# Optimization experiments

Measured on AMD Instinct MI355X. Metric: run time of the kernel, lower is better.

The kernel has to match this reference:

```python
import jax, jax.numpy as jnp
import numpy as np

N, E, D, H = 100000, 1250000, 64, 128
EPS = 1e-5


def sage_bn_relu(x, src, dst, W_self, b_self, W_neigh, gamma, beta):
    # mean aggregation over in-neighbors (DGL SAGEConv 'mean')
    n = x.shape[0]
    deg = jax.ops.segment_sum(jnp.ones((src.shape[0],), x.dtype), dst, num_segments=n)
    agg = jax.ops.segment_sum(x[src], dst, num_segments=n)  # [N, d]
    neigh = agg / jnp.maximum(deg, 1.0)[:, None]             # zero in-degree -> 0
    h = x @ W_self + b_self + neigh @ W_neigh                # fc_self + fc_neigh
    # BatchNorm1d (training-mode batch statistics, biased variance)
    mu = h.mean(0)
    var = jnp.mean((h - mu) ** 2, axis=0)
    h = (h - mu) * jax.lax.rsqrt(var + EPS) * gamma + beta
    return jax.nn.relu(h)  # dropout omitted (deterministic eval)


def setup_inputs() -> dict:
    key = jax.random.key(0)
    ks = jax.random.split(key, 32)
    inp = {
        "x": jax.random.normal(ks[0], (N, D), jnp.float32),
        "src": jax.random.randint(ks[1], (E,), 0, N),
        "dst": jax.random.randint(ks[2], (E,), 0, N),
    }
    dims = [(D, H), (H, H), (H, H)]
    k = 3
    for i, (din, dout) in enumerate(dims):
        s = 1.0 / np.sqrt(din)
        inp[f"W_self{i}"] = jax.random.uniform(ks[k], (din, dout), jnp.float32, -s, s); k += 1
        inp[f"b_self{i}"] = jnp.zeros((dout,), jnp.float32)
        inp[f"W_neigh{i}"] = jax.random.uniform(ks[k], (din, dout), jnp.float32, -s, s); k += 1
        inp[f"gamma{i}"] = jnp.ones((dout,), jnp.float32)
        inp[f"beta{i}"] = jnp.zeros((dout,), jnp.float32)
    s = 1.0 / np.sqrt(H)
    inp["Wc"] = jax.random.uniform(ks[k], (H, 2), jnp.float32, -s, s)
    inp["bc"] = jnp.zeros((2,), jnp.float32)
    return inp


def reference(x, src, dst,
              W_self0, b_self0, W_neigh0, gamma0, beta0,
              W_self1, b_self1, W_neigh1, gamma1, beta1,
              W_self2, b_self2, W_neigh2, gamma2, beta2,
              Wc, bc):
    h = sage_bn_relu(x, src, dst, W_self0, b_self0, W_neigh0, gamma0, beta0)
    h = sage_bn_relu(h, src, dst, W_self1, b_self1, W_neigh1, gamma1, beta1)
    h = sage_bn_relu(h, src, dst, W_self2, b_self2, W_neigh2, gamma2, beta2)
    return h @ Wc + bc  # [N, 2]
```

## Files before the change

kernel.cpp:

```cpp
#include <hip/hip_runtime.h>


#define N_NODES 100000
#define N_EDGES 1250000
#define NB 1024
#define BSZ 98
#define CAP 1536
#define BPART 256
#define INVN (1.0f / 100000.0f)

typedef short bf16x8 __attribute__((ext_vector_type(8)));
typedef float f32x4 __attribute__((ext_vector_type(4)));
typedef unsigned short u16x8 __attribute__((ext_vector_type(8)));
typedef unsigned short u16x4 __attribute__((ext_vector_type(4)));

__device__ __forceinline__ float bf2f(unsigned short u) {
  union { unsigned int i; float f; } c; c.i = ((unsigned int)u) << 16; return c.f;
}
__device__ __forceinline__ unsigned short f2bf(float f) {
  union { float f; unsigned int i; } c; c.f = f;
  unsigned int r = (c.i + 0x7FFFu + ((c.i >> 16) & 1u)) >> 16;
  return (unsigned short)r;
}
__device__ __forceinline__ void bn_st(const float* stats, const float* gam,
                                      const float* bet, int c, float& s, float& t) {
  float sum = stats[c] + stats[256 + c] + stats[512 + c] + stats[768 + c];
  float sq  = stats[128 + c] + stats[384 + c] + stats[640 + c] + stats[896 + c];
  float mu = sum * INVN;
  float var = sq * INVN - mu * mu;
  s = gam[c] * rsqrtf(var + 1e-5f);
  t = bet[c] - mu * s;
}
__device__ __forceinline__ void gload_lds16(const void* g, void* l) {
  __builtin_amdgcn_global_load_lds(
      (const __attribute__((address_space(1))) unsigned int*)g,
      (__attribute__((address_space(3))) unsigned int*)l, 16, 0, 0);
}

__global__ __launch_bounds__(256) void k_prep(
    const float* __restrict__ x, unsigned short* __restrict__ x16,
    const float* __restrict__ W0s, const float* __restrict__ W0n,
    const float* __restrict__ W1s, const float* __restrict__ W1n,
    const float* __restrict__ W2s, const float* __restrict__ W2n,
    unsigned short* __restrict__ wt, float* __restrict__ stats3,
    const int* __restrict__ dst, int* __restrict__ hist, int E) {
  __shared__ int hh[NB];
  int blk = blockIdx.x, t = threadIdx.x;
  if (blk < 6250) {
    int i = blk * 256 + t;
    float4 v = ((const float4*)x)[i];
    u16x4 o;
    o.x = f2bf(v.x); o.y = f2bf(v.y); o.z = f2bf(v.z); o.w = f2bf(v.w);
    ((u16x4*)x16)[i] = o;
  } else if (blk < 6570) {
    int i = (blk - 6250) * 256 + t;
    if (i < 16384) {
      const float* W = (i < 8192) ? W0s : W0n;
      unsigned short* o = wt + (i < 8192 ? 0 : 8192);
      int j = i & 8191;
      int c = j >> 6, k = j & 63;
      o[j] = f2bf(W[k * 128 + c]);
    } else {
      int j = i - 16384;
      int sel = j >> 14;
      j &= 16383;
      const float* W = (sel == 0) ? W1s : (sel == 1) ? W1n : (sel == 2) ? W2s : W2n;
      unsigned short* o = wt + 16384 + sel * 16384;
      int c = j >> 7, k = j & 127;
      o[j] = f2bf(W[k * 128 + c]);
    }
  } else if (blk == 6570) {
    for (int i = t; i < 3 * 1024; i += 256) stats3[i] = 0.f;
  } else {
    int hb = blk - 6571;
    int chunk = (E + BPART - 1) / BPART;
    int start = hb * chunk;
    int end = min(E, start + chunk);
    for (int b = t; b < NB; b += 256) hh[b] = 0;
    __syncthreads();
    for (int e = start + t; e < end; e += 256) atomicAdd(&hh[dst[e] / BSZ], 1);
    __syncthreads();
    for (int b = t; b < NB; b += 256) hist[hb * NB + b] = hh[b];
  }
}

__global__ __launch_bounds__(256) void k_scan(const int* __restrict__ hist,
                                              int* __restrict__ base,
                                              int* __restrict__ gcursor) {
  int bb = blockIdx.x * 256 + threadIdx.x;
  if (bb >= NB) return;
  int run = 0;
  for (int r0 = 0; r0 < BPART; r0 += 16) {
    int v[16];
    #pragma unroll
    for (int u = 0; u < 16; u++) v[u] = hist[(r0 + u) * NB + bb];
    #pragma unroll
    for (int u = 0; u < 16; u++) { base[(r0 + u) * NB + bb] = run; run += v[u]; }
  }
  gcursor[bb] = run;
}

__global__ __launch_bounds__(256) void k_scatter(const int* __restrict__ src,
                                                 const int* __restrict__ dst,
                                                 const int* __restrict__ base,
                                                 unsigned int* __restrict__ part, int E) {
  __shared__ int cur[NB];
  int t = threadIdx.x;
  int chunk = (E + BPART - 1) / BPART;
  int start = blockIdx.x * chunk;
  int end = min(E, start + chunk);
  for (int b = t; b < NB; b += 256) cur[b] = base[blockIdx.x * NB + b];
  __syncthreads();
  for (int e = start + t; e < end; e += 256) {
    int d = dst[e];
    int b = d / BSZ;
    int pos = atomicAdd(&cur[b], 1);
    if ((unsigned)pos < (unsigned)CAP)
      part[(size_t)b * CAP + pos] = (unsigned)src[e] | ((unsigned)(d - b * BSZ) << 17);
  }
}

template <int DIM>
__global__ __launch_bounds__(512) void k_aggb(const unsigned short* __restrict__ h,
                                              const unsigned int* __restrict__ part,
                                              const int* __restrict__ gcursor,
                                              unsigned short* __restrict__ neigh, int n,
                                              const float* __restrict__ statsP,
                                              const float* __restrict__ gamP,
                                              const float* __restrict__ betP) {
  __shared__ unsigned eraw[CAP];
  __shared__ unsigned eord[CAP];
  __shared__ int cnt[BSZ], offv[BSZ], cur[BSZ];
  __shared__ int scan[128];
  int t = threadIdx.x;
  int bkt = blockIdx.x;
  int node0 = bkt * BSZ;
  int nn = min(BSZ, n - node0);
  if (nn <= 0) return;
  if (t < BSZ) cnt[t] = 0;
  __syncthreads();
  int ec = gcursor[bkt];
  ec = max(0, min(ec, CAP));
  for (int i = t; i < ec; i += 512) {
    unsigned w = part[(size_t)bkt * CAP + i];
    eraw[i] = w;
    atomicAdd(&cnt[w >> 17], 1);
  }
  __syncthreads();
  if (t < 128) scan[t] = (t < BSZ) ? cnt[t] : 0;
  __syncthreads();
  #pragma unroll
  for (int o = 1; o < 128; o <<= 1) {
    int x = 0;
    if (t < 128 && t >= o) x = scan[t - o];
    __syncthreads();
    if (t < 128) scan[t] += x;
    __syncthreads();
  }
  if (t < BSZ) { offv[t] = scan[t] - cnt[t]; cur[t] = scan[t] - cnt[t]; }
  __syncthreads();
  for (int i = t; i < ec; i += 512) {
    unsigned w = eraw[i];
    int p = atomicAdd(&cur[w >> 17], 1);
    eord[p] = w & 0x1FFFF;
  }
  __syncthreads();
  const int G = DIM / 8, NG = 512 / G;
  int gid = t / G, li = t % G;
  float sreg[8], treg[8];
  bool bn = (statsP != nullptr);
  if (bn) {
    #pragma unroll
    for (int k = 0; k < 8; k++) bn_st(statsP, gamP, betP, li * 8 + k, sreg[k], treg[k]);
  }
  for (int nd = gid; nd < nn; nd += NG) {
    int s = offv[nd], c = cnt[nd];
    int e = s + c;
    float acc[8] = {0.f, 0.f, 0.f, 0.f, 0.f, 0.f, 0.f, 0.f};
    int j = s;
    for (; j + 2 <= e; j += 2) {
      int sn0 = eord[j], sn1 = eord[j + 1];
      u16x8 v0 = *(const u16x8*)&h[(size_t)sn0 * DIM + li * 8];
      u16x8 v1 = *(const u16x8*)&h[(size_t)sn1 * DIM + li * 8];
      if (bn) {
        #pragma unroll
        for (int k = 0; k < 8; k++)
          acc[k] += fmaxf(fmaf(bf2f(v0[k]), sreg[k], treg[k]), 0.f)
                  + fmaxf(fmaf(bf2f(v1[k]), sreg[k], treg[k]), 0.f);
      } else {
        #pragma unroll
        for (int k = 0; k < 8; k++) acc[k] += bf2f(v0[k]) + bf2f(v1[k]);
      }
    }
    if (j < e) {
      int sn = eord[j];
      u16x8 v = *(const u16x8*)&h[(size_t)sn * DIM + li * 8];
      if (bn) {
        #pragma unroll
        for (int k = 0; k < 8; k++)
          acc[k] += fmaxf(fmaf(bf2f(v[k]), sreg[k], treg[k]), 0.f);
      } else {
        #pragma unroll
        for (int k = 0; k < 8; k++) acc[k] += bf2f(v[k]);
      }
    }
    float inv = 1.0f / fmaxf((float)c, 1.0f);
    u16x8 o;
    #pragma unroll
    for (int k = 0; k < 8; k++) o[k] = f2bf(acc[k] * inv);
    *(u16x8*)&neigh[(size_t)(node0 + nd) * DIM + li * 8] = o;
  }
}

__global__ __launch_bounds__(256) void k_gemm_mfma(
    const unsigned short* __restrict__ A1, const unsigned short* __restrict__ W1t,
    const unsigned short* __restrict__ A2, const unsigned short* __restrict__ W2t,
    const float* __restrict__ bias, unsigned short* __restrict__ C,
    float* __restrict__ stats, int M, int din,
    const float* __restrict__ statsP, const float* __restrict__ gamP,
    const float* __restrict__ betP) {
  __shared__ unsigned short As[2][128 * 32];
  __shared__ unsigned short Bs[2][128 * 32];
  __shared__ float redS[4 * 128];
  __shared__ float redQ[4 * 128];
  __shared__ float sBN[128], tBN[128];

  int t = threadIdx.x;
  int lane = t & 63, w = t >> 6;
  int l15 = lane & 15, quad = lane >> 4;
  int row0 = blockIdx.x * 128;
  bool hasBN = (statsP != nullptr);
  if (hasBN && t < 128) bn_st(statsP, gamP, betP, t, sBN[t], tBN[t]);
  if (hasBN) __syncthreads();

  const int steps1 = din >> 5;
  const int S = steps1 * 2;

  f32x4 acc[2][8];
  #pragma unroll
  for (int rt = 0; rt < 2; rt++)
    #pragma unroll
    for (int ct = 0; ct < 8; ct++) acc[rt][ct] = (f32x4){0.f, 0.f, 0.f, 0.f};

  auto Aof  = [&](int s) { return (s < steps1) ? A1 : A2; };
  auto Wof  = [&](int s) { return (s < steps1) ? W1t : W2t; };
  auto k0of = [&](int s) { return ((s < steps1) ? s : s - steps1) << 5; };

  auto stageA = [&](int s, int bi) {
    const unsigned short* A = Aof(s); int k0 = k0of(s);
    #pragma unroll
    for (int i = 0; i < 2; i++) {
      int idx = t + 256 * i;
      int r = idx >> 2, prt = idx & 3;
      gload_lds16(&A[(size_t)(row0 + r) * din + k0 + prt * 8],
                  &As[bi][(i * 256 + w * 64) * 8]);
    }
  };
  auto stageB = [&](int s, int bi) {
    const unsigned short* Wt = Wof(s); int k0 = k0of(s);
    #pragma unroll
    for (int i = 0; i < 2; i++) {
      int idx = t + 256 * i;
      int r = idx >> 2, prt = idx & 3;
      gload_lds16(&Wt[(size_t)r * din + k0 + prt * 8],
                  &Bs[bi][(i * 256 + w * 64) * 8]);
    }
  };
  u16x8 vreg[2];
  auto bnLoad = [&](int s) {
    const unsigned short* A = Aof(s); int k0 = k0of(s);
    #pragma unroll
    for (int i = 0; i < 2; i++) {
      int idx = t + 256 * i;
      int r = idx >> 2, prt = idx & 3;
      vreg[i] = *(const u16x8*)&A[(size_t)(row0 + r) * din + k0 + prt * 8];
    }
  };
  auto bnWrite = [&](int s, int bi) {
    int k0 = k0of(s);
    #pragma unroll
    for (int i = 0; i < 2; i++) {
      int idx = t + 256 * i;
      int prt = idx & 3;
      u16x8 v = vreg[i];
      #pragma unroll
      for (int j = 0; j < 8; j++) {
        int c = k0 + prt * 8 + j;
        v[j] = f2bf(fmaxf(fmaf(bf2f(v[j]), sBN[c], tBN[c]), 0.f));
      }
      *(u16x8*)&As[bi][idx * 8] = v;
    }
  };

  if (hasBN) { bnLoad(0); stageB(0, 0); bnWrite(0, 0); }
  else       { stageA(0, 0); stageB(0, 0); }
  __syncthreads();

  int cb = 0;
  for (int s = 0; s < S; s++) {
    int nb = cb ^ 1;
    bool haveNext = (s + 1 < S);
    bool bnNext = hasBN && (s + 1 < steps1);
    if (haveNext) {
      if (bnNext) bnLoad(s + 1);
      else        stageA(s + 1, nb);
      stageB(s + 1, nb);
    }
    bf16x8 af[2], bfr[8];
    #pragma unroll
    for (int rt = 0; rt < 2; rt++)
      af[rt] = *(const bf16x8*)&As[cb][(w * 32 + rt * 16 + l15) * 32 + quad * 8];
    #pragma unroll
    for (int ct = 0; ct < 8; ct++)
      bfr[ct] = *(const bf16x8*)&Bs[cb][(ct * 16 + l15) * 32 + quad * 8];
    #pragma unroll
    for (int rt = 0; rt < 2; rt++)
      #pragma unroll
      for (int ct = 0; ct < 8; ct++)
        acc[rt][ct] = __builtin_amdgcn_mfma_f32_16x16x32_bf16(af[rt], bfr[ct], acc[rt][ct], 0, 0, 0);
    if (haveNext) {
      if (bnNext) bnWrite(s + 1, nb);
      __syncthreads();
    }
    cb = nb;
  }

  float bcol[8], ls[8], lq[8];
  #pragma unroll
  for (int ct = 0; ct < 8; ct++) {
    bcol[ct] = bias[ct * 16 + l15];
    ls[ct] = 0.f; lq[ct] = 0.f;
  }
  #pragma unroll
  for (int rt = 0; rt < 2; rt++) {
    #pragma unroll
    for (int r = 0; r < 4; r++) {
      int row = row0 + w * 32 + rt * 16 + quad * 4 + r;
      if (row < M) {
        #pragma unroll
        for (int ct = 0; ct < 8; ct++) {
          float v = acc[rt][ct][r] + bcol[ct];
          C[(size_t)row * 128 + ct * 16 + l15] = f2bf(v);
          ls[ct] += v; lq[ct] += v * v;
        }
      }
    }
  }
  #pragma unroll
  for (int ct = 0; ct < 8; ct++) {
    ls[ct] += __shfl_xor(ls[ct], 16); ls[ct] += __shfl_xor(ls[ct], 32);
    lq[ct] += __shfl_xor(lq[ct], 16); lq[ct] += __shfl_xor(lq[ct], 32);
  }
  if (quad == 0) {
    #pragma unroll
    for (int ct = 0; ct < 8; ct++) {
      redS[w * 128 + ct * 16 + l15] = ls[ct];
      redQ[w * 128 + ct * 16 + l15] = lq[ct];
    }
  }
  __syncthreads();
  if (t < 128) {
    float s = redS[t] + redS[128 + t] + redS[256 + t] + redS[384 + t];
    float q = redQ[t] + redQ[128 + t] + redQ[256 + t] + redQ[384 + t];
    int rep = (blockIdx.x & 3) * 256;
    atomicAdd(&stats[rep + t], s);
    atomicAdd(&stats[rep + 128 + t], q);
  }
}

__global__ void k_final(const unsigned short* __restrict__ h,
                        const float* __restrict__ statsP, const float* __restrict__ gamP,
                        const float* __restrict__ betP, const float* __restrict__ Wc,
                        const float* __restrict__ bc, float* __restrict__ out, int n) {
  int lane = threadIdx.x & 63;
  int row = blockIdx.x * (blockDim.x >> 6) + (threadIdx.x >> 6);
  if (row >= n) return;
  float acc0 = 0.f, acc1 = 0.f;
  #pragma unroll
  for (int m = 0; m < 2; m++) {
    int c = lane + 64 * m;
    float s, tt;
    bn_st(statsP, gamP, betP, c, s, tt);
    float v = bf2f(h[(size_t)row * 128 + c]);
    v = fmaxf(fmaf(v, s, tt), 0.f);
    acc0 += v * Wc[c * 2 + 0];
    acc1 += v * Wc[c * 2 + 1];
  }
  #pragma unroll
  for (int off = 32; off > 0; off >>= 1) {
    acc0 += __shfl_down(acc0, off);
    acc1 += __shfl_down(acc1, off);
  }
  if (lane == 0) {
    out[row * 2 + 0] = acc0 + bc[0];
    out[row * 2 + 1] = acc1 + bc[1];
  }
}

extern "C" void kernel_launch(void* const* d_in, const int* in_sizes, int n_in,
                              void* d_out, int out_size, void* d_ws, size_t ws_size,
                              hipStream_t stream) {
  const float* x   = (const float*)d_in[0];
  const int* src   = (const int*)d_in[1];
  const int* dst   = (const int*)d_in[2];
  const float* Wself[3] = {(const float*)d_in[3], (const float*)d_in[8],  (const float*)d_in[13]};
  const float* bself[3] = {(const float*)d_in[4], (const float*)d_in[9],  (const float*)d_in[14]};
  const float* Wngh[3]  = {(const float*)d_in[5], (const float*)d_in[10], (const float*)d_in[15]};
  const float* gam[3]   = {(const float*)d_in[6], (const float*)d_in[11], (const float*)d_in[16]};
  const float* bet[3]   = {(const float*)d_in[7], (const float*)d_in[12], (const float*)d_in[17]};
  const float* Wc = (const float*)d_in[18];
  const float* bc = (const float*)d_in[19];
  float* out = (float*)d_out;

  const int N = N_NODES, E = N_EDGES;

  unsigned short* x16 = (unsigned short*)d_ws;
  unsigned short* b0  = x16 + (size_t)N * 64;
  unsigned short* b1  = b0 + (size_t)N * 128;
  unsigned short* b2  = b1 + (size_t)N * 128;
  unsigned short* wt  = b2 + (size_t)N * 128;
  unsigned int* part  = (unsigned int*)(wt + 81920);
  int* gcursor  = (int*)(part + (size_t)NB * CAP);
  float* stats3 = (float*)(gcursor + NB);

  int* hist = (int*)b1;
  int* base = hist + (size_t)BPART * NB;

  k_prep<<<6571 + BPART, 256, 0, stream>>>(x, x16, Wself[0], Wngh[0], Wself[1],
                                           Wngh[1], Wself[2], Wngh[2], wt, stats3,
                                           dst, hist, E);

  k_scan<<<(NB + 255) / 256, 256, 0, stream>>>(hist, base, gcursor);
  k_scatter<<<BPART, 256, 0, stream>>>(src, dst, base, part, E);

  const int gemmBlocks = (N + 127) / 128;

  k_aggb<64><<<NB, 512, 0, stream>>>(x16, part, gcursor, b0, N,
                                     nullptr, nullptr, nullptr);
  k_gemm_mfma<<<gemmBlocks, 256, 0, stream>>>(x16, wt + 0, b0, wt + 8192, bself[0],
                                              b1, stats3 + 0, N, 64,
                                              nullptr, nullptr, nullptr);

  k_aggb<128><<<NB, 512, 0, stream>>>(b1, part, gcursor, b0, N,
                                      stats3 + 0, gam[0], bet[0]);
  k_gemm_mfma<<<gemmBlocks, 256, 0, stream>>>(b1, wt + 16384, b0, wt + 32768, bself[1],
                                              b2, stats3 + 1024, N, 128,
                                              stats3 + 0, gam[0], bet[0]);

  k_aggb<128><<<NB, 512, 0, stream>>>(b2, part, gcursor, b0, N,
                                      stats3 + 1024, gam[1], bet[1]);
  k_gemm_mfma<<<gemmBlocks, 256, 0, stream>>>(b2, wt + 49152, b0, wt + 65536, bself[2],
                                              b1, stats3 + 2048, N, 128,
                                              stats3 + 1024, gam[1], bet[1]);

  k_final<<<(N + 3) / 4, 256, 0, stream>>>(b1, stats3 + 2048, gam[2], bet[2],
                                           Wc, bc, out, N);
}
```

Baseline: 390.8 us.

## Rebalance bucket sizes, grid-stride prep conversion, dynamic node stealing in aggregation

The bucket size drops to 96 nodes, which gives 1042 buckets, and the partition count doubles to 512 so each histogram/scatter block handles fewer edges. The x-to-bf16 conversion in the prep kernel now uses a fixed pool of blocks with a grid-stride loop instead of one block per chunk. In the aggregation kernel, each thread group claims its next node from a shared-memory atomic counter instead of using a static stride, to even out the skewed per-node edge counts. The risks are an extra LDS atomic and shuffle per node, a larger histogram and scan workload, and hard-coded constants elsewhere, such as the BN stats layout, that may assume NB=1024.

```diff
diff --git a/kernel.cpp b/kernel.cpp
--- a/kernel.cpp
+++ b/kernel.cpp
@@ -3,10 +3,11 @@
 
 #define N_NODES 100000
 #define N_EDGES 1250000
-#define NB 1024
-#define BSZ 98
+#define NB 1042
+#define BSZ 96
 #define CAP 1536
-#define BPART 256
+#define BPART 512
+#define PREP_X 1024
 #define INVN (1.0f / 100000.0f)
 
 typedef short bf16x8 __attribute__((ext_vector_type(8)));
@@ -46,14 +47,15 @@
     const int* __restrict__ dst, int* __restrict__ hist, int E) {
   __shared__ int hh[NB];
   int blk = blockIdx.x, t = threadIdx.x;
-  if (blk < 6250) {
-    int i = blk * 256 + t;
-    float4 v = ((const float4*)x)[i];
-    u16x4 o;
-    o.x = f2bf(v.x); o.y = f2bf(v.y); o.z = f2bf(v.z); o.w = f2bf(v.w);
-    ((u16x4*)x16)[i] = o;
-  } else if (blk < 6570) {
-    int i = (blk - 6250) * 256 + t;
+  if (blk < PREP_X) {
+    for (int i = blk * 256 + t; i < N_NODES * 16; i += PREP_X * 256) {
+      float4 v = ((const float4*)x)[i];
+      u16x4 o;
+      o.x = f2bf(v.x); o.y = f2bf(v.y); o.z = f2bf(v.z); o.w = f2bf(v.w);
+      ((u16x4*)x16)[i] = o;
+    }
+  } else if (blk < PREP_X + 320) {
+    int i = (blk - PREP_X) * 256 + t;
     if (i < 16384) {
       const float* W = (i < 8192) ? W0s : W0n;
       unsigned short* o = wt + (i < 8192 ? 0 : 8192);
@@ -69,10 +71,10 @@
       int c = j >> 7, k = j & 127;
       o[j] = f2bf(W[k * 128 + c]);
     }
-  } else if (blk == 6570) {
+  } else if (blk == PREP_X + 320) {
     for (int i = t; i < 3 * 1024; i += 256) stats3[i] = 0.f;
   } else {
-    int hb = blk - 6571;
+    int hb = blk - (PREP_X + 321);
     int chunk = (E + BPART - 1) / BPART;
     int start = hb * chunk;
     int end = min(E, start + chunk);
@@ -132,12 +134,14 @@
   __shared__ unsigned eord[CAP];
   __shared__ int cnt[BSZ], offv[BSZ], cur[BSZ];
   __shared__ int scan[128];
+  __shared__ int stealCtr;
   int t = threadIdx.x;
   int bkt = blockIdx.x;
   int node0 = bkt * BSZ;
   int nn = min(BSZ, n - node0);
   if (nn <= 0) return;
   if (t < BSZ) cnt[t] = 0;
+  if (t == 0) stealCtr = 0;
   __syncthreads();
   int ec = gcursor[bkt];
   ec = max(0, min(ec, CAP));
@@ -165,15 +169,19 @@
     eord[p] = w & 0x1FFFF;
   }
   __syncthreads();
-  const int G = DIM / 8, NG = 512 / G;
-  int gid = t / G, li = t % G;
+  const int G = DIM / 8;
+  int li = t % G;
   float sreg[8], treg[8];
   bool bn = (statsP != nullptr);
   if (bn) {
     #pragma unroll
     for (int k = 0; k < 8; k++) bn_st(statsP, gamP, betP, li * 8 + k, sreg[k], treg[k]);
   }
-  for (int nd = gid; nd < nn; nd += NG) {
+  for (;;) {
+    int nd0 = 0;
+    if (li == 0) nd0 = atomicAdd(&stealCtr, 1);
+    int nd = __shfl(nd0, 0, G);
+    if (nd >= nn) break;
     int s = offv[nd], c = cnt[nd];
     int e = s + c;
     float acc[8] = {0.f, 0.f, 0.f, 0.f, 0.f, 0.f, 0.f, 0.f};
@@ -426,9 +434,9 @@
   int* hist = (int*)b1;
   int* base = hist + (size_t)BPART * NB;
 
-  k_prep<<<6571 + BPART, 256, 0, stream>>>(x, x16, Wself[0], Wngh[0], Wself[1],
-                                           Wngh[1], Wself[2], Wngh[2], wt, stats3,
-                                           dst, hist, E);
+  k_prep<<<PREP_X + 321 + BPART, 256, 0, stream>>>(
+      x, x16, Wself[0], Wngh[0], Wself[1], Wngh[1], Wself[2], Wngh[2],
+      wt, stats3, dst, hist, E);
 
   k_scan<<<(NB + 255) / 256, 256, 0, stream>>>(hist, base, gcursor);
   k_scatter<<<BPART, 256, 0, stream>>>(src, dst, base, part, E);
```

Result: slower. 401.5 us (+2.7%).
